# Kernel tuning notes

Measured on AMD Instinct MI355X. Metric: run time of the kernel, lower is better.

Reference implementation:

```python
import jax, jax.numpy as jnp
from jax import lax
import numpy as np

N_BLOCKS = 5; C = 256; K = 1024; NQ = 8; NRES = 4; B = 2; T = 65536


def conv1d(x, w, b, stride=1, padding=0, dilation=1):
    # x: [N,C,T], w: [O,I,k]
    y = lax.conv_general_dilated(x, w, (stride,), [(padding, padding)],
                                 rhs_dilation=(dilation,),
                                 dimension_numbers=('NCH', 'OIH', 'NCH'))
    return y + b[None, :, None]


def conv_transpose1d(x, w, b):
    # PyTorch ConvTranspose1d(k=4, s=2, p=1); w: [in, out, 4]
    wk = jnp.swapaxes(jnp.flip(w, -1), 0, 1)  # [out, in, 4]
    y = lax.conv_general_dilated(x, wk, (1,), [(2, 2)], lhs_dilation=(2,),
                                 dimension_numbers=('NCH', 'OIH', 'NCH'))
    return y + b[None, :, None]


def residual_model(x, w0, b0, w1, b1, dil):
    # ReLU -> dilated conv3 -> ReLU -> conv3
    h = conv1d(jax.nn.relu(x), w0, b0, padding=dil, dilation=dil)
    h = conv1d(jax.nn.relu(h), w1, b1, padding=1)
    return h


def encoder(x, d0w, d0b, dw, db, rw, rb):
    for i in range(N_BLOCKS):
        if i == 0:
            x = conv1d(x, d0w, d0b, stride=2, padding=1)
        else:
            x = conv1d(x, dw[i - 1], db[i - 1], stride=2, padding=1)
        for j in range(NRES):
            dil = 3 ** (j + 1)
            # ResidualBlock.forward: x + model(x)
            x = x + residual_model(x, rw[i, j, 0], rb[i, j, 0], rw[i, j, 1], rb[i, j, 1], dil)
    return x


def decoder(x, rw, rb, uw, ub, ulw, ulb):
    for i in range(N_BLOCKS):
        for j in range(NRES):
            dil = 3 ** (j + 1)
            # DecoderBlock: x = x + ResidualBlock(x) = x + (x + model(x))
            x = x + (x + residual_model(x, rw[i, j, 0], rb[i, j, 0], rw[i, j, 1], rb[i, j, 1], dil))
        if i == N_BLOCKS - 1:
            x = conv_transpose1d(x, ulw, ulb)
        else:
            x = conv_transpose1d(x, uw[i], ub[i])
    return x


def rvq(emb, rvq_sum, rvq_usage):
    # emb: [N, C]; eval-mode residual VQ (no EMA update)
    q = jnp.zeros_like(emb)
    commit = jnp.asarray(0.0, emb.dtype)
    codes = []
    for i in range(NQ):
        cb = rvq_sum[i] / jnp.clip(rvq_usage[i], 1e-5, None)[:, None]  # [K, C]
        res = emb - q
        # argmin of squared distance over codebook rows (||res||^2 constant per column)
        scores = jnp.sum(cb * cb, axis=1)[:, None] - 2.0 * (cb @ res.T)  # [K, N]
        c = jnp.argmin(scores, axis=0)
        eq = cb[c]  # [N, C]
        eq_st = res + lax.stop_gradient(eq - res)  # straight-through
        commit = commit + jnp.mean((lax.stop_gradient(eq_st) - res) ** 2)
        q = q + eq_st
        codes.append(c.astype(jnp.int32))
    return jnp.stack(codes, axis=1), q, commit


def setup_inputs() -> dict:
    key = jax.random.key(0)
    ks = iter(jax.random.split(key, 16))

    def W(shape, fan_in):
        return (jax.random.normal(next(ks), shape, jnp.float32) / np.float32(np.sqrt(fan_in)))

    return {
        'x': jax.random.normal(next(ks), (B, 1, T), jnp.float32),
        'enc_down0_w': W((C, 1, 4), 4),
        'enc_down0_b': jnp.zeros((C,), jnp.float32),
        'enc_down_w': W((N_BLOCKS - 1, C, C, 4), C * 4),
        'enc_down_b': jnp.zeros((N_BLOCKS - 1, C), jnp.float32),
        'enc_res_w': W((N_BLOCKS, NRES, 2, C, C, 3), C * 3),
        'enc_res_b': jnp.zeros((N_BLOCKS, NRES, 2, C), jnp.float32),
        'dec_res_w': W((N_BLOCKS, NRES, 2, C, C, 3), C * 3),
        'dec_res_b': jnp.zeros((N_BLOCKS, NRES, 2, C), jnp.float32),
        'dec_up_w': W((N_BLOCKS - 1, C, C, 4), C * 4),
        'dec_up_b': jnp.zeros((N_BLOCKS - 1, C), jnp.float32),
        'dec_up_last_w': W((C, 1, 4), C * 4),
        'dec_up_last_b': jnp.zeros((1,), jnp.float32),
        'rvq_sum': jax.random.normal(next(ks), (NQ, K, C), jnp.float32) * 0.1,
        'rvq_usage': jnp.ones((NQ, K), jnp.float32),
    }


def reference(x, enc_down0_w, enc_down0_b, enc_down_w, enc_down_b, enc_res_w, enc_res_b,
              dec_res_w, dec_res_b, dec_up_w, dec_up_b, dec_up_last_w, dec_up_last_b,
              rvq_sum, rvq_usage):
    z = encoder(x, enc_down0_w, enc_down0_b, enc_down_w, enc_down_b, enc_res_w, enc_res_b)
    Bz, Cz, Tz = z.shape
    emb = jnp.transpose(z, (0, 2, 1)).reshape(Bz * Tz, Cz)  # (b t) c
    codes, q, commit = rvq(emb, rvq_sum, rvq_usage)
    zq = jnp.transpose(q.reshape(Bz, Tz, Cz), (0, 2, 1))  # b c t
    recon = decoder(zq, dec_res_w, dec_res_b, dec_up_w, dec_up_b, dec_up_last_w, dec_up_last_b)
    return recon, codes, commit
```

## Files before the change

kernel.cpp:

```cpp
#include <hip/hip_runtime.h>
#include <cstdint>

#define DEVFN static __device__ __forceinline__
typedef unsigned short ushort_t;
typedef unsigned int uint_t;
typedef short short8 __attribute__((ext_vector_type(8)));
typedef float f32x4 __attribute__((ext_vector_type(4)));

DEVFN float bf2f(ushort_t h) { return __uint_as_float(((uint_t)h) << 16); }
DEVFN ushort_t bfhi(float f) {
    uint_t u = __float_as_uint(f);
    u += 0x7fffu + ((u >> 16) & 1u);
    return (ushort_t)(u >> 16);
}
DEVFN void fsplit(float f, ushort_t& h, ushort_t& l) {
    h = bfhi(f);
    l = bfhi(f - bf2f(h));
}
DEVFN void relu_pair(uint_t& h, uint_t& l) {
    float f0 = bf2f((ushort_t)(h & 0xffffu)) + bf2f((ushort_t)(l & 0xffffu));
    float f1 = bf2f((ushort_t)(h >> 16)) + bf2f((ushort_t)(l >> 16));
    if (f0 <= 0.f) { h &= 0xffff0000u; l &= 0xffff0000u; }
    if (f1 <= 0.f) { h &= 0x0000ffffu; l &= 0x0000ffffu; }
}
DEVFN int xcd_swz(int bx, int gx) {
    return ((gx & 7) == 0) ? ((bx & 7) * (gx >> 3) + (bx >> 3)) : bx;
}

__global__ __launch_bounds__(256)
void wprep3_k(const float* __restrict__ erw, const float* __restrict__ drw,
              ushort_t* __restrict__ wH, ushort_t* __restrict__ wL)
{
    const int gid = blockIdx.x * 256 + threadIdx.x;
    const int conv = gid >> 16;
    const int rem  = gid & 65535;
    const int co = rem >> 8, ci = rem & 255;
    const float* src = (conv < 40) ? (erw + (size_t)conv * 196608)
                                   : (drw + (size_t)(conv - 40) * 196608);
    const float* p = src + ((size_t)co * 256 + ci) * 3;
    ushort_t* oh = wH + (size_t)conv * 196608 + rem;
    ushort_t* ol = wL + (size_t)conv * 196608 + rem;
#pragma unroll
    for (int k = 0; k < 3; ++k) {
        ushort_t h, l; fsplit(p[k], h, l);
        oh[k * 65536] = h; ol[k * 65536] = l;
    }
}

__global__ __launch_bounds__(256)
void wprep4_k(const float* __restrict__ edw, const float* __restrict__ duw,
              ushort_t* __restrict__ wH, ushort_t* __restrict__ wL)
{
    const int gid = blockIdx.x * 256 + threadIdx.x;
    const int conv = gid >> 16;
    const int rem  = gid & 65535;
    const int co = rem >> 8, ci = rem & 255;
    ushort_t* oh = wH + (size_t)conv * 262144 + rem;
    ushort_t* ol = wL + (size_t)conv * 262144 + rem;
#pragma unroll
    for (int k = 0; k < 4; ++k) {
        float f;
        if (conv < 4)  f = edw[(size_t)conv * 262144 + ((size_t)co * 256 + ci) * 4 + k];
        else           f = duw[(size_t)(conv - 4) * 262144 + ((size_t)ci * 256 + co) * 4 + k];
        ushort_t h, l; fsplit(f, h, l);
        oh[k * 65536] = h; ol[k * 65536] = l;
    }
}

template<int TAPS, int STRIDE, bool RELU, int NT, int DMAX, bool DBUF>
__global__ __launch_bounds__(256, (NT >= 8) ? 2 : 3)
void convs_k(const ushort_t* __restrict__ inH, const ushort_t* __restrict__ inL,
             const ushort_t* __restrict__ wH, const ushort_t* __restrict__ wL,
             const float* __restrict__ bias,
             const ushort_t* __restrict__ srcH, const ushort_t* __restrict__ srcL,
             float alpha,
             ushort_t* __restrict__ outH, ushort_t* __restrict__ outL,
             int Lin, int Lout, int dil, int pad)
{
    constexpr int ROWS = NT * 16;
    constexpr int SMAX = STRIDE * (ROWS - 1) + (TAPS - 1) * DMAX + 1;
    constexpr int XSB  = SMAX * 80;
    constexpr int NEED = DBUF ? 4 * XSB : 2 * XSB;
    constexpr int EMIN = (NT >= 2) ? 33280 : 16640;
    constexpr int ARENA = (NEED > EMIN) ? NEED : EMIN;
    static_assert(!DBUF || (4 * SMAX <= TAPS * 256), "prefetch item budget");
    __shared__ __align__(16) char sarena[ARENA];

    const int tid = threadIdx.x;
    const int b = blockIdx.z;
    const int t0 = xcd_swz(blockIdx.x, gridDim.x) * ROWS;
    const int wave = tid >> 6, lane = tid & 63;
    const int quad = lane >> 4, lr = lane & 15;
    const int cow = wave * 64;
    const size_t inbase = (size_t)b * Lin * 256;
    const int S = STRIDE * (ROWS - 1) + (TAPS - 1) * dil + 1;
    const int g0 = STRIDE * t0 - pad;

    f32x4 acc[4][NT];
#pragma unroll
    for (int m = 0; m < 4; ++m)
#pragma unroll
        for (int n = 0; n < NT; ++n) acc[m][n] = (f32x4)0.f;

    if constexpr (DBUF) {
        ushort_t (*xsH0)[40] = (ushort_t(*)[40])(sarena);
        ushort_t (*xsL0)[40] = (ushort_t(*)[40])(sarena + XSB);
        ushort_t (*xsH1)[40] = (ushort_t(*)[40])(sarena + 2 * XSB);
        ushort_t (*xsL1)[40] = (ushort_t(*)[40])(sarena + 3 * XSB);
        for (int idx = tid; idx < S * 4; idx += 256) {
            const int s = idx >> 2, p = idx & 3;
            const int t = g0 + s;
            uint4 hv = make_uint4(0, 0, 0, 0), lv = hv;
            if (t >= 0 && t < Lin) {
                const size_t g = inbase + (size_t)t * 256 + p * 8;
                hv = *(const uint4*)(inH + g);
                lv = *(const uint4*)(inL + g);
                if (RELU) {
                    relu_pair(hv.x, lv.x); relu_pair(hv.y, lv.y);
                    relu_pair(hv.z, lv.z); relu_pair(hv.w, lv.w);
                }
            }
            *(uint4*)&xsH0[s][p * 8] = hv;
            *(uint4*)&xsL0[s][p * 8] = lv;
        }
        __syncthreads();
        for (int chunk = 0; chunk < 8; ++chunk) {
            const int ci0 = chunk * 32;
            ushort_t (*xsH)[40] = (chunk & 1) ? xsH1 : xsH0;
            ushort_t (*xsL)[40] = (chunk & 1) ? xsL1 : xsL0;
            ushort_t (*xnH)[40] = (chunk & 1) ? xsH0 : xsH1;
            ushort_t (*xnL)[40] = (chunk & 1) ? xsL0 : xsL1;
            const bool pf = (chunk < 7);
#pragma unroll
            for (int tap = 0; tap < TAPS; ++tap) {
                const ushort_t* wHt = wH + (size_t)tap * 65536 + ci0 + quad * 8;
                const ushort_t* wLt = wL + (size_t)tap * 65536 + ci0 + quad * 8;
                short8 aH[4], aL[4];
#pragma unroll
                for (int m = 0; m < 4; ++m) {
                    const int co = cow + m * 16 + lr;
                    aH[m] = *(const short8*)(wHt + co * 256);
                    aL[m] = *(const short8*)(wLt + co * 256);
                }
                const int idx = tap * 256 + tid;
                const int s = idx >> 2, p = idx & 3;
                const int tr = g0 + s;
                const bool inr = (idx < S * 4);
                uint4 hv = make_uint4(0, 0, 0, 0), lv = hv;
                if (pf && inr && tr >= 0 && tr < Lin) {
                    const size_t g = inbase + (size_t)tr * 256 + (ci0 + 32) + p * 8;
                    hv = *(const uint4*)(inH + g);
                    lv = *(const uint4*)(inL + g);
                }
                const int rb = tap * dil;
                __builtin_amdgcn_s_setprio(1);
#pragma unroll
                for (int n = 0; n < NT; ++n) {
                    const int srow = STRIDE * (n * 16 + lr) + rb;
                    const short8 bH = *(const short8*)&xsH[srow][quad * 8];
                    const short8 bL = *(const short8*)&xsL[srow][quad * 8];
#pragma unroll
                    for (int m = 0; m < 4; ++m)
                        acc[m][n] = __builtin_amdgcn_mfma_f32_16x16x32_bf16(aH[m], bH, acc[m][n], 0, 0, 0);
#pragma unroll
                    for (int m = 0; m < 4; ++m)
                        acc[m][n] = __builtin_amdgcn_mfma_f32_16x16x32_bf16(aH[m], bL, acc[m][n], 0, 0, 0);
#pragma unroll
                    for (int m = 0; m < 4; ++m)
                        acc[m][n] = __builtin_amdgcn_mfma_f32_16x16x32_bf16(aL[m], bH, acc[m][n], 0, 0, 0);
                }
                __builtin_amdgcn_s_setprio(0);
                if (pf && inr) {
                    if (RELU) {
                        relu_pair(hv.x, lv.x); relu_pair(hv.y, lv.y);
                        relu_pair(hv.z, lv.z); relu_pair(hv.w, lv.w);
                    }
                    *(uint4*)&xnH[s][p * 8] = hv;
                    *(uint4*)&xnL[s][p * 8] = lv;
                }
            }
            __syncthreads();
        }
    } else {
        ushort_t (*xsH)[40] = (ushort_t(*)[40])(sarena);
        ushort_t (*xsL)[40] = (ushort_t(*)[40])(sarena + XSB);
        for (int chunk = 0; chunk < 8; ++chunk) {
            const int ci0 = chunk * 32;
            __syncthreads();
            for (int idx = tid; idx < S * 4; idx += 256) {
                const int s = idx >> 2, p = idx & 3;
                const int t = g0 + s;
                uint4 hv = make_uint4(0, 0, 0, 0), lv = hv;
                if (t >= 0 && t < Lin) {
                    const size_t g = inbase + (size_t)t * 256 + ci0 + p * 8;
                    hv = *(const uint4*)(inH + g);
                    lv = *(const uint4*)(inL + g);
                    if (RELU) {
                        relu_pair(hv.x, lv.x); relu_pair(hv.y, lv.y);
                        relu_pair(hv.z, lv.z); relu_pair(hv.w, lv.w);
                    }
                }
                *(uint4*)&xsH[s][p * 8] = hv;
                *(uint4*)&xsL[s][p * 8] = lv;
            }
            __syncthreads();
#pragma unroll
            for (int tap = 0; tap < TAPS; ++tap) {
                const ushort_t* wHt = wH + (size_t)tap * 65536 + ci0 + quad * 8;
                const ushort_t* wLt = wL + (size_t)tap * 65536 + ci0 + quad * 8;
                short8 aH[4], aL[4];
#pragma unroll
                for (int m = 0; m < 4; ++m) {
                    const int co = cow + m * 16 + lr;
                    aH[m] = *(const short8*)(wHt + co * 256);
                    aL[m] = *(const short8*)(wLt + co * 256);
                }
                const int rb = tap * dil;
                __builtin_amdgcn_s_setprio(1);
#pragma unroll
                for (int n = 0; n < NT; ++n) {
                    const int srow = STRIDE * (n * 16 + lr) + rb;
                    const short8 bH = *(const short8*)&xsH[srow][quad * 8];
                    const short8 bL = *(const short8*)&xsL[srow][quad * 8];
#pragma unroll
                    for (int m = 0; m < 4; ++m)
                        acc[m][n] = __builtin_amdgcn_mfma_f32_16x16x32_bf16(aH[m], bH, acc[m][n], 0, 0, 0);
#pragma unroll
                    for (int m = 0; m < 4; ++m)
                        acc[m][n] = __builtin_amdgcn_mfma_f32_16x16x32_bf16(aH[m], bL, acc[m][n], 0, 0, 0);
#pragma unroll
                    for (int m = 0; m < 4; ++m)
                        acc[m][n] = __builtin_amdgcn_mfma_f32_16x16x32_bf16(aL[m], bH, acc[m][n], 0, 0, 0);
                }
                __builtin_amdgcn_s_setprio(0);
            }
        }
    }
    float4 bvv[4];
#pragma unroll
    for (int m = 0; m < 4; ++m)
        bvv[m] = *(const float4*)&bias[cow + m * 16 + quad * 4];
    __syncthreads();
    if constexpr (NT >= 2) {
        float (*ebuf)[260] = (float(*)[260])sarena;
#pragma unroll
        for (int n2 = 0; n2 < NT; n2 += 2) {
#pragma unroll
            for (int half = 0; half < 2; ++half) {
                const int n = n2 + half;
#pragma unroll
                for (int m = 0; m < 4; ++m) {
                    float4 v;
                    v.x = acc[m][n][0] + bvv[m].x;
                    v.y = acc[m][n][1] + bvv[m].y;
                    v.z = acc[m][n][2] + bvv[m].z;
                    v.w = acc[m][n][3] + bvv[m].w;
                    *(float4*)&ebuf[16 * half + lr][cow + m * 16 + quad * 4] = v;
                }
            }
            __syncthreads();
#pragma unroll
            for (int h = 0; h < 8; ++h) {
                const int row = (tid >> 4) + 16 * (h >> 2);
                const int col = (tid & 15) * 4 + (h & 3) * 64;
                const int t = t0 + n2 * 16 + row;
                const size_t gr = ((size_t)b * Lout + t) * 256;
                float4 v = *(const float4*)&ebuf[row][col];
                if (alpha != 0.f) {
                    const ushort4 sh = *(const ushort4*)(srcH + gr + col);
                    const ushort4 sl = *(const ushort4*)(srcL + gr + col);
                    v.x += alpha * (bf2f(sh.x) + bf2f(sl.x));
                    v.y += alpha * (bf2f(sh.y) + bf2f(sl.y));
                    v.z += alpha * (bf2f(sh.z) + bf2f(sl.z));
                    v.w += alpha * (bf2f(sh.w) + bf2f(sl.w));
                }
                ushort4 oh, ol;
                fsplit(v.x, oh.x, ol.x); fsplit(v.y, oh.y, ol.y);
                fsplit(v.z, oh.z, ol.z); fsplit(v.w, oh.w, ol.w);
                *(ushort4*)(outH + gr + col) = oh;
                *(ushort4*)(outL + gr + col) = ol;
            }
            __syncthreads();
        }
    } else {
        float (*ebuf)[260] = (float(*)[260])sarena;
#pragma unroll
        for (int n = 0; n < NT; ++n) {
#pragma unroll
            for (int m = 0; m < 4; ++m) {
                float4 v;
                v.x = acc[m][n][0] + bvv[m].x;
                v.y = acc[m][n][1] + bvv[m].y;
                v.z = acc[m][n][2] + bvv[m].z;
                v.w = acc[m][n][3] + bvv[m].w;
                *(float4*)&ebuf[lr][cow + m * 16 + quad * 4] = v;
            }
            __syncthreads();
            {
                const int row = tid >> 4;
                const int c00 = (tid & 15) * 4;
                const int t = t0 + n * 16 + row;
                const size_t gr = ((size_t)b * Lout + t) * 256;
#pragma unroll
                for (int rep = 0; rep < 4; ++rep) {
                    const int col = c00 + rep * 64;
                    float4 v = *(const float4*)&ebuf[row][col];
                    if (alpha != 0.f) {
                        const ushort4 sh = *(const ushort4*)(srcH + gr + col);
                        const ushort4 sl = *(const ushort4*)(srcL + gr + col);
                        v.x += alpha * (bf2f(sh.x) + bf2f(sl.x));
                        v.y += alpha * (bf2f(sh.y) + bf2f(sl.y));
                        v.z += alpha * (bf2f(sh.z) + bf2f(sl.z));
                        v.w += alpha * (bf2f(sh.w) + bf2f(sl.w));
                    }
                    ushort4 oh, ol;
                    fsplit(v.x, oh.x, ol.x); fsplit(v.y, oh.y, ol.y);
                    fsplit(v.z, oh.z, ol.z); fsplit(v.w, oh.w, ol.w);
                    *(ushort4*)(outH + gr + col) = oh;
                    *(ushort4*)(outL + gr + col) = ol;
                }
            }
            __syncthreads();
        }
    }
}

template<int NTc>
__global__ __launch_bounds__(256, 2)
void convt_k(const ushort_t* __restrict__ inH, const ushort_t* __restrict__ inL,
             const ushort_t* __restrict__ wH, const ushort_t* __restrict__ wL,
             const float* __restrict__ bias,
             ushort_t* __restrict__ outH, ushort_t* __restrict__ outL, int Lin)
{
    constexpr int ROWS = NTc * 16;
    constexpr int S = ROWS + 2;
    constexpr int XSB = S * 40 * 2;
    constexpr int ARENA = (2 * XSB > 33280) ? 2 * XSB : 33280;
    __shared__ __align__(16) char sarena[ARENA];
    ushort_t (*xsH)[40] = (ushort_t(*)[40])(sarena);
    ushort_t (*xsL)[40] = (ushort_t(*)[40])(sarena + XSB);

    const int tid = threadIdx.x;
    const int b = blockIdx.z;
    const int m0 = xcd_swz(blockIdx.x, gridDim.x) * ROWS;
    const int Lout = Lin * 2;
    const int wave = tid >> 6, lane = tid & 63;
    const int quad = lane >> 4, lr = lane & 15;
    const int cow = wave * 64;
    const size_t inbase = (size_t)b * Lin * 256;

    f32x4 acc[4][NTc][2];
#pragma unroll
    for (int m = 0; m < 4; ++m)
#pragma unroll
        for (int n = 0; n < NTc; ++n) { acc[m][n][0] = (f32x4)0.f; acc[m][n][1] = (f32x4)0.f; }

    for (int chunk = 0; chunk < 8; ++chunk) {
        const int ci0 = chunk * 32;
        __syncthreads();
        for (int idx = tid; idx < S * 4; idx += 256) {
            const int s = idx >> 2, p = idx & 3;
            const int t = m0 - 1 + s;
            uint4 hv = make_uint4(0, 0, 0, 0), lv = hv;
            if (t >= 0 && t < Lin) {
                const size_t g = inbase + (size_t)t * 256 + ci0 + p * 8;
                hv = *(const uint4*)(inH + g);
                lv = *(const uint4*)(inL + g);
            }
            *(uint4*)&xsH[s][p * 8] = hv;
            *(uint4*)&xsL[s][p * 8] = lv;
        }
        __syncthreads();
#pragma unroll
        for (int tap = 0; tap < 4; ++tap) {
            const int ph = (tap == 0 || tap == 2) ? 1 : 0;
            const int sh = (tap == 0) ? 1 : ((tap == 3) ? -1 : 0);
            const ushort_t* wHt = wH + (size_t)tap * 65536 + ci0 + quad * 8;
            const ushort_t* wLt = wL + (size_t)tap * 65536 + ci0 + quad * 8;
            short8 aH[4], aL[4];
#pragma unroll
            for (int m = 0; m < 4; ++m) {
                const int co = cow + m * 16 + lr;
                aH[m] = *(const short8*)(wHt + co * 256);
                aL[m] = *(const short8*)(wLt + co * 256);
            }
            __builtin_amdgcn_s_setprio(1);
#pragma unroll
            for (int n = 0; n < NTc; ++n) {
                const int srow = n * 16 + lr + sh + 1;
                const short8 bH = *(const short8*)&xsH[srow][quad * 8];
                const short8 bL = *(const short8*)&xsL[srow][quad * 8];
#pragma unroll
                for (int m = 0; m < 4; ++m)
                    acc[m][n][ph] = __builtin_amdgcn_mfma_f32_16x16x32_bf16(aH[m], bH, acc[m][n][ph], 0, 0, 0);
#pragma unroll
                for (int m = 0; m < 4; ++m)
                    acc[m][n][ph] = __builtin_amdgcn_mfma_f32_16x16x32_bf16(aH[m], bL, acc[m][n][ph], 0, 0, 0);
#pragma unroll
                for (int m = 0; m < 4; ++m)
                    acc[m][n][ph] = __builtin_amdgcn_mfma_f32_16x16x32_bf16(aL[m], bH, acc[m][n][ph], 0, 0, 0);
            }
            __builtin_amdgcn_s_setprio(0);
        }
    }
    float4 bvv[4];
#pragma unroll
    for (int m = 0; m < 4; ++m)
        bvv[m] = *(const float4*)&bias[cow + m * 16 + quad * 4];
    __syncthreads();
    float (*ebuf)[260] = (float(*)[260])sarena;
#pragma unroll
    for (int n = 0; n < NTc; ++n) {
#pragma unroll
        for (int m = 0; m < 4; ++m) {
#pragma unroll
            for (int ph = 0; ph < 2; ++ph) {
                float4 v;
                v.x = acc[m][n][ph][0] + bvv[m].x;
                v.y = acc[m][n][ph][1] + bvv[m].y;
                v.z = acc[m][n][ph][2] + bvv[m].z;
                v.w = acc[m][n][ph][3] + bvv[m].w;
                *(float4*)&ebuf[2 * lr + ph][cow + m * 16 + quad * 4] = v;
            }
        }
        __syncthreads();
        {
            const int baset = 2 * (m0 + n * 16);
#pragma unroll
            for (int h = 0; h < 8; ++h) {
                const int row = (tid >> 4) + 16 * (h >> 2);
                const int col = (tid & 15) * 4 + (h & 3) * 64;
                const int t = baset + row;
                const size_t gr = ((size_t)b * Lout + t) * 256 + col;
                float4 v = *(const float4*)&ebuf[row][col];
                ushort4 oh, ol;
                fsplit(v.x, oh.x, ol.x); fsplit(v.y, oh.y, ol.y);
                fsplit(v.z, oh.z, ol.z); fsplit(v.w, oh.w, ol.w);
                *(ushort4*)(outH + gr) = oh;
                *(ushort4*)(outL + gr) = ol;
            }
        }
        __syncthreads();
    }
}

__global__ __launch_bounds__(256)
void down0_k2(const float* __restrict__ x, const float* __restrict__ w,
              const float* __restrict__ bias,
              ushort_t* __restrict__ outH, ushort_t* __restrict__ outL)
{
    const int t = blockIdx.x;
    const int b = blockIdx.y;
    const int co = threadIdx.x;
    const float* xb = x + (size_t)b * 65536;
    const float4 wv = *(const float4*)(w + co * 4);
    float s = bias[co];
    const int ti0 = 2 * t - 1;
    if (ti0 >= 0)      s = fmaf(xb[ti0], wv.x, s);
    s = fmaf(xb[ti0 + 1], wv.y, s);
    s = fmaf(xb[ti0 + 2], wv.z, s);
    if (ti0 + 3 < 65536) s = fmaf(xb[ti0 + 3], wv.w, s);
    ushort_t h, l; fsplit(s, h, l);
    const size_t g = ((size_t)b * 32768 + t) * 256 + co;
    outH[g] = h; outL[g] = l;
}

__global__ __launch_bounds__(256)
void uplast_k2(const ushort_t* __restrict__ inH, const ushort_t* __restrict__ inL,
               const float* __restrict__ w, const float* __restrict__ bias,
               float* __restrict__ out, int Lin)
{
    const int m = blockIdx.x * 256 + threadIdx.x;
    const int b = blockIdx.y;
    const float bv = bias[0];
    float aE = bv, aO = bv;
    const size_t base = (size_t)b * Lin * 256;
    const ushort_t* r0H = inH + base + (size_t)m * 256;
    const ushort_t* r0L = inL + base + (size_t)m * 256;
    const bool hasM = (m > 0), hasP = (m + 1 < Lin);
    for (int c0 = 0; c0 < 256; c0 += 8) {
        uint4 h0 = *(const uint4*)(r0H + c0);
        uint4 l0 = *(const uint4*)(r0L + c0);
        uint4 hm = make_uint4(0,0,0,0), lm = hm, hp = hm, lp = hm;
        if (hasM) { hm = *(const uint4*)(r0H - 256 + c0); lm = *(const uint4*)(r0L - 256 + c0); }
        if (hasP) { hp = *(const uint4*)(r0H + 256 + c0); lp = *(const uint4*)(r0L + 256 + c0); }
        const uint_t* h0p = (const uint_t*)&h0; const uint_t* l0p = (const uint_t*)&l0;
        const uint_t* hmp = (const uint_t*)&hm; const uint_t* lmp = (const uint_t*)&lm;
        const uint_t* hpp = (const uint_t*)&hp; const uint_t* lpp = (const uint_t*)&lp;
#pragma unroll
        for (int e = 0; e < 4; ++e) {
#pragma unroll
            for (int half = 0; half < 2; ++half) {
                const int sh = half * 16;
                const int ci = c0 + e * 2 + half;
                const float x0  = bf2f((ushort_t)(h0p[e] >> sh)) + bf2f((ushort_t)(l0p[e] >> sh));
                const float xm1 = bf2f((ushort_t)(hmp[e] >> sh)) + bf2f((ushort_t)(lmp[e] >> sh));
                const float xp1 = bf2f((ushort_t)(hpp[e] >> sh)) + bf2f((ushort_t)(lpp[e] >> sh));
                const float4 wv = *(const float4*)(w + ci * 4);
                aE = fmaf(x0, wv.y, fmaf(xm1, wv.w, aE));
                aO = fmaf(xp1, wv.x, fmaf(x0, wv.z, aO));
            }
        }
    }
    *(float2*)(out + (size_t)b * 2 * Lin + 2 * m) = make_float2(aE, aO);
}

__global__ void emb_k(const ushort_t* __restrict__ H, const ushort_t* __restrict__ L,
                      float* __restrict__ emb)
{
    const size_t g = (size_t)blockIdx.x * 256 + threadIdx.x;
    emb[g] = bf2f(H[g]) + bf2f(L[g]);
}
__global__ void qsplit_k(const float* __restrict__ q,
                         ushort_t* __restrict__ H, ushort_t* __restrict__ L)
{
    const size_t g = (size_t)blockIdx.x * 256 + threadIdx.x;
    ushort_t h, l; fsplit(q[g], h, l);
    H[g] = h; L[g] = l;
}

__global__ __launch_bounds__(256)
void rvq_cb_all_k(const float* __restrict__ sum, const float* __restrict__ usage,
                  float* __restrict__ cb, float* __restrict__ cbT,
                  float* __restrict__ cbn)
{
    const int k = blockIdx.x, iq = blockIdx.y, c = threadIdx.x;
    const float den = fmaxf(usage[iq * 1024 + k], 1e-5f);
    const float v = sum[((size_t)iq * 1024 + k) * 256 + c] / den;
    cb[(size_t)iq * 262144 + (size_t)k * 256 + c] = v;
    cbT[(size_t)iq * 262144 + (size_t)c * 1024 + k] = v;
    float s = v * v;
    for (int off = 32; off; off >>= 1) s += __shfl_down(s, off, 64);
    __shared__ float ls[4];
    if ((c & 63) == 0) ls[c >> 6] = s;
    __syncthreads();
    if (c == 0) cbn[iq * 1024 + k] = ls[0] + ls[1] + ls[2] + ls[3];
}

DEVFN unsigned int ordbits(float f)
{
    unsigned u = __float_as_uint(f);
    return (u & 0x80000000u) ? ~u : (u | 0x80000000u);
}
DEVFN unsigned long long shfl_xor_u64(unsigned long long v, int mask)
{
    int lo = (int)(v & 0xffffffffull), hi = (int)(v >> 32);
    lo = __shfl_xor(lo, mask, 64);
    hi = __shfl_xor(hi, mask, 64);
    return ((unsigned long long)(unsigned)hi << 32) | (unsigned)lo;
}

__global__ __launch_bounds__(256)
void rvq_argmin_upd_k(const float* __restrict__ emb, float* __restrict__ q,
                      const float* __restrict__ cb, const float* __restrict__ cbT,
                      const float* __restrict__ cbn,
                      int* __restrict__ codes, float* __restrict__ codes_out,
                      float* __restrict__ commit, int iq)
{
    cb  += (size_t)iq * 262144;
    cbT += (size_t)iq * 262144;
    cbn += (size_t)iq * 1024;
    const int n0 = blockIdx.x * 16;
    const int tid = threadIdx.x;
    __shared__ float res[16][256];
    for (int idx = tid; idx < 16 * 256; idx += 256) {
        int nl = idx >> 8, c = idx & 255;
        size_t g = (size_t)(n0 + nl) * 256 + c;
        res[nl][c] = emb[g] - q[g];
    }
    __syncthreads();
    float dot[16][4];
#pragma unroll
    for (int nl = 0; nl < 16; ++nl)
#pragma unroll
        for (int j = 0; j < 4; ++j) dot[nl][j] = 0.f;

    const float* cbtp = cbT + tid * 4;
    for (int c = 0; c < 256; ++c) {
        const float4 cbv = *(const float4*)(cbtp + (size_t)c * 1024);
#pragma unroll
        for (int nl = 0; nl < 16; ++nl) {
            const float r = res[nl][c];
            dot[nl][0] = fmaf(cbv.x, r, dot[nl][0]);
            dot[nl][1] = fmaf(cbv.y, r, dot[nl][1]);
            dot[nl][2] = fmaf(cbv.z, r, dot[nl][2]);
            dot[nl][3] = fmaf(cbv.w, r, dot[nl][3]);
        }
    }
    const float4 nrm = *(const float4*)(cbn + tid * 4);
    __shared__ unsigned long long wred[4][16];
    __shared__ int scode[16];
    const int wave = tid >> 6, lane = tid & 63;
#pragma unroll
    for (int nl = 0; nl < 16; ++nl) {
        float s0 = nrm.x - 2.f * dot[nl][0];
        float s1 = nrm.y - 2.f * dot[nl][1];
        float s2 = nrm.z - 2.f * dot[nl][2];
        float s3 = nrm.w - 2.f * dot[nl][3];
        unsigned long long key =
            ((unsigned long long)ordbits(s0) << 32) | (unsigned)(tid * 4 + 0);
        unsigned long long k1 =
            ((unsigned long long)ordbits(s1) << 32) | (unsigned)(tid * 4 + 1);
        unsigned long long k2 =
            ((unsigned long long)ordbits(s2) << 32) | (unsigned)(tid * 4 + 2);
        unsigned long long k3 =
            ((unsigned long long)ordbits(s3) << 32) | (unsigned)(tid * 4 + 3);
        if (k1 < key) key = k1;
        if (k2 < key) key = k2;
        if (k3 < key) key = k3;
        for (int off = 32; off; off >>= 1) {
            unsigned long long o = shfl_xor_u64(key, off);
            if (o < key) key = o;
        }
        if (lane == 0) wred[wave][nl] = key;
    }
    __syncthreads();
    if (tid < 16) {
        unsigned long long bkey = wred[0][tid];
        if (wred[1][tid] < bkey) bkey = wred[1][tid];
        if (wred[2][tid] < bkey) bkey = wred[2][tid];
        if (wred[3][tid] < bkey) bkey = wred[3][tid];
        const int code = (int)(bkey & 0xffffffffull);
        scode[tid] = code;
        codes[(size_t)(n0 + tid) * 8 + iq] = code;
        codes_out[(size_t)(n0 + tid) * 8 + iq] = (float)code;
    }
    __syncthreads();
    float csum = 0.f;
#pragma unroll 4
    for (int nl = 0; nl < 16; ++nl) {
        const int code = scode[nl];
        const float cbv = cb[(size_t)code * 256 + tid];
        const float r = res[nl][tid];
        const size_t g = (size_t)(n0 + nl) * 256 + tid;
        q[g] = emb[g] - r + cbv;
        const float e = cbv - r;
        csum = fmaf(e, e, csum);
    }
    for (int off = 32; off; off >>= 1) csum += __shfl_down(csum, off, 64);
    __shared__ float ls2[4];
    if ((tid & 63) == 0) ls2[tid >> 6] = csum;
    __syncthreads();
    if (tid == 0) atomicAdd(commit, ls2[0] + ls2[1] + ls2[2] + ls2[3]);
}

__global__ void commit_write_k(const float* __restrict__ commit, float* __restrict__ out)
{
    out[0] = commit[0] * (1.f / (4096.f * 256.f));
}

extern "C" void kernel_launch(void* const* d_in, const int* in_sizes, int n_in,
                              void* d_out, int out_size, void* d_ws, size_t ws_size,
                              hipStream_t stream)
{
    const float* x    = (const float*)d_in[0];
    const float* ed0w = (const float*)d_in[1];
    const float* ed0b = (const float*)d_in[2];
    const float* edw  = (const float*)d_in[3];
    const float* edb  = (const float*)d_in[4];
    const float* erw  = (const float*)d_in[5];
    const float* erb  = (const float*)d_in[6];
    const float* drw  = (const float*)d_in[7];
    const float* drb  = (const float*)d_in[8];
    const float* duw  = (const float*)d_in[9];
    const float* dub  = (const float*)d_in[10];
    const float* dulw = (const float*)d_in[11];
    const float* dulb = (const float*)d_in[12];
    const float* rsum = (const float*)d_in[13];
    const float* rusg = (const float*)d_in[14];
    float* out = (float*)d_out;

    char* base = (char*)d_ws;
    size_t o = 0;
    ushort_t* wH3 = (ushort_t*)(base + o); o += 31457280;
    ushort_t* wL3 = (ushort_t*)(base + o); o += 31457280;
    ushort_t* w4H = (ushort_t*)(base + o); o += 4194304;
    ushort_t* w4L = (ushort_t*)(base + o); o += 4194304;
    ushort_t* AH  = (ushort_t*)(base + o); o += 33554432;
    ushort_t* AL  = (ushort_t*)(base + o); o += 33554432;
    ushort_t* BH  = (ushort_t*)(base + o); o += 33554432;
    ushort_t* BL  = (ushort_t*)(base + o); o += 33554432;
    float* emb    = (float*)(base + o);    o += 4194304;
    float* q      = (float*)(base + o);    o += 4194304;
    float* commit = (float*)(base + o);    o += 64;
    float* cb     = (float*)(base + o);    o += 8388608;
    float* cbT    = (float*)(base + o);    o += 8388608;
    float* cbn    = (float*)(base + o);    o += 32768;
    int*   codes  = (int*)(base + o);      o += 131072;

    static const int DIL[4] = {3, 9, 27, 81};

    hipMemsetAsync(q, 0, 4194304 + 64, stream);

    wprep3_k<<<20480, 256, 0, stream>>>(erw, drw, wH3, wL3);
    wprep4_k<<<2048, 256, 0, stream>>>(edw, duw, w4H, w4L);

    auto conv3 = [&](const ushort_t* iH, const ushort_t* iL,
                     const ushort_t* wh, const ushort_t* wl, const float* bb,
                     const ushort_t* sH, const ushort_t* sL, float alpha,
                     ushort_t* oH, ushort_t* oL, int L, int d) {
        const bool db = (d <= 27);
        if (L >= 16384) {
            if (db) convs_k<3, 1, true, 8, 27, true><<<dim3(L / 128, 1, 2), 256, 0, stream>>>(
                        iH, iL, wh, wl, bb, sH, sL, alpha, oH, oL, L, L, d, d);
            else    convs_k<3, 1, true, 8, 81, false><<<dim3(L / 128, 1, 2), 256, 0, stream>>>(
                        iH, iL, wh, wl, bb, sH, sL, alpha, oH, oL, L, L, d, d);
        } else if (L >= 8192) {
            if (db) convs_k<3, 1, true, 4, 27, true><<<dim3(L / 64, 1, 2), 256, 0, stream>>>(
                        iH, iL, wh, wl, bb, sH, sL, alpha, oH, oL, L, L, d, d);
            else    convs_k<3, 1, true, 4, 81, false><<<dim3(L / 64, 1, 2), 256, 0, stream>>>(
                        iH, iL, wh, wl, bb, sH, sL, alpha, oH, oL, L, L, d, d);
        } else if (L >= 4096) {
            if (db) convs_k<3, 1, true, 2, 27, true><<<dim3(L / 32, 1, 2), 256, 0, stream>>>(
                        iH, iL, wh, wl, bb, sH, sL, alpha, oH, oL, L, L, d, d);
            else    convs_k<3, 1, true, 2, 81, false><<<dim3(L / 32, 1, 2), 256, 0, stream>>>(
                        iH, iL, wh, wl, bb, sH, sL, alpha, oH, oL, L, L, d, d);
        } else {
            if (db) convs_k<3, 1, true, 1, 27, true><<<dim3(L / 16, 1, 2), 256, 0, stream>>>(
                        iH, iL, wh, wl, bb, sH, sL, alpha, oH, oL, L, L, d, d);
            else    convs_k<3, 1, true, 1, 81, false><<<dim3(L / 16, 1, 2), 256, 0, stream>>>(
                        iH, iL, wh, wl, bb, sH, sL, alpha, oH, oL, L, L, d, d);
        }
    };

    down0_k2<<<dim3(32768, 2), 256, 0, stream>>>(x, ed0w, ed0b, AH, AL);
    int L = 32768;
    for (int i = 0; i < 5; ++i) {
        if (i > 0) {
            const ushort_t* wh = w4H + (size_t)(i - 1) * 262144;
            const ushort_t* wl = w4L + (size_t)(i - 1) * 262144;
            const int Lout = L / 2;
            if (Lout >= 16384)
                convs_k<4, 2, false, 8, 1, false><<<dim3(Lout / 128, 1, 2), 256, 0, stream>>>(
                    AH, AL, wh, wl, edb + (i - 1) * 256, AH, AL, 0.f, BH, BL, L, Lout, 1, 1);
            else if (Lout >= 8192)
                convs_k<4, 2, false, 4, 1, false><<<dim3(Lout / 64, 1, 2), 256, 0, stream>>>(
                    AH, AL, wh, wl, edb + (i - 1) * 256, AH, AL, 0.f, BH, BL, L, Lout, 1, 1);
            else if (Lout >= 4096)
                convs_k<4, 2, false, 2, 1, false><<<dim3(Lout / 32, 1, 2), 256, 0, stream>>>(
                    AH, AL, wh, wl, edb + (i - 1) * 256, AH, AL, 0.f, BH, BL, L, Lout, 1, 1);
            else
                convs_k<4, 2, false, 1, 1, false><<<dim3(Lout / 16, 1, 2), 256, 0, stream>>>(
                    AH, AL, wh, wl, edb + (i - 1) * 256, AH, AL, 0.f, BH, BL, L, Lout, 1, 1);
            ushort_t* t;
            t = AH; AH = BH; BH = t;
            t = AL; AL = BL; BL = t;
            L = Lout;
        }
        for (int j = 0; j < 4; ++j) {
            const int d = DIL[j];
            const size_t u = (size_t)(i * 4 + j) * 2;
            conv3(AH, AL, wH3 + (u + 0) * 196608, wL3 + (u + 0) * 196608,
                  erb + (u + 0) * 256, AH, AL, 0.f, BH, BL, L, d);
            conv3(BH, BL, wH3 + (u + 1) * 196608, wL3 + (u + 1) * 196608,
                  erb + (u + 1) * 256, AH, AL, 1.f, AH, AL, L, 1);
        }
    }

    emb_k<<<4096, 256, 0, stream>>>(AH, AL, emb);
    rvq_cb_all_k<<<dim3(1024, 8), 256, 0, stream>>>(rsum, rusg, cb, cbT, cbn);
    for (int iq = 0; iq < 8; ++iq) {
        rvq_argmin_upd_k<<<256, 256, 0, stream>>>(emb, q, cb, cbT, cbn,
                                                  codes, out + 131072, commit, iq);
    }
    qsplit_k<<<4096, 256, 0, stream>>>(q, AH, AL);

    L = 2048;
    for (int i = 0; i < 5; ++i) {
        for (int j = 0; j < 4; ++j) {
            const int d = DIL[j];
            const size_t u = 40 + (size_t)(i * 4 + j) * 2;
            conv3(AH, AL, wH3 + (u + 0) * 196608, wL3 + (u + 0) * 196608,
                  drb + ((size_t)(i * 4 + j) * 2 + 0) * 256, AH, AL, 0.f, BH, BL, L, d);
            conv3(BH, BL, wH3 + (u + 1) * 196608, wL3 + (u + 1) * 196608,
                  drb + ((size_t)(i * 4 + j) * 2 + 1) * 256, AH, AL, 2.f, AH, AL, L, 1);
        }
        if (i < 4) {
            const ushort_t* wh = w4H + (size_t)(4 + i) * 262144;
            const ushort_t* wl = w4L + (size_t)(4 + i) * 262144;
            if (L >= 8192)
                convt_k<4><<<dim3(L / 64, 1, 2), 256, 0, stream>>>(
                    AH, AL, wh, wl, dub + i * 256, BH, BL, L);
            else if (L >= 4096)
                convt_k<2><<<dim3(L / 32, 1, 2), 256, 0, stream>>>(
                    AH, AL, wh, wl, dub + i * 256, BH, BL, L);
            else
                convt_k<1><<<dim3(L / 16, 1, 2), 256, 0, stream>>>(
                    AH, AL, wh, wl, dub + i * 256, BH, BL, L);
            ushort_t* t;
            t = AH; AH = BH; BH = t;
            t = AL; AL = BL; BL = t;
            L *= 2;
        } else {
            uplast_k2<<<dim3(L / 256, 2), 256, 0, stream>>>(AH, AL, dulw, dulb, out, L);
        }
    }

    commit_write_k<<<1, 1, 0, stream>>>(commit, out + 163840);
}
```

Measured before the change: 5.277 ms.

## Fuse all RVQ stages into one kernel keeping residual in shared memory

Replaces the emb conversion kernel, the eight per-stage argmin/update launches and the q split kernel with a single kernel that loads the encoder output once, keeps the residual and quantized accumulator in shared memory across all eight codebook stages, and writes the split bf16 pair back at the end. This removes the repeated global reads and writes of emb and q and nine kernel launches. It also changes the dilated conv3 dispatch so the small-dilation variant uses the 8-wide tile only at L>=32768 and the 4-wide tile at 16384. Shared memory per block doubles, and the 32-bit codes buffer is no longer written.

```diff
diff --git a/kernel.cpp b/kernel.cpp
--- a/kernel.cpp
+++ b/kernel.cpp
@@ -505,20 +505,6 @@
     *(float2*)(out + (size_t)b * 2 * Lin + 2 * m) = make_float2(aE, aO);
 }
 
-__global__ void emb_k(const ushort_t* __restrict__ H, const ushort_t* __restrict__ L,
-                      float* __restrict__ emb)
-{
-    const size_t g = (size_t)blockIdx.x * 256 + threadIdx.x;
-    emb[g] = bf2f(H[g]) + bf2f(L[g]);
-}
-__global__ void qsplit_k(const float* __restrict__ q,
-                         ushort_t* __restrict__ H, ushort_t* __restrict__ L)
-{
-    const size_t g = (size_t)blockIdx.x * 256 + threadIdx.x;
-    ushort_t h, l; fsplit(q[g], h, l);
-    H[g] = h; L[g] = l;
-}
-
 __global__ __launch_bounds__(256)
 void rvq_cb_all_k(const float* __restrict__ sum, const float* __restrict__ usage,
                   float* __restrict__ cb, float* __restrict__ cbT,
@@ -551,97 +537,114 @@
 }
 
 __global__ __launch_bounds__(256)
-void rvq_argmin_upd_k(const float* __restrict__ emb, float* __restrict__ q,
-                      const float* __restrict__ cb, const float* __restrict__ cbT,
-                      const float* __restrict__ cbn,
-                      int* __restrict__ codes, float* __restrict__ codes_out,
-                      float* __restrict__ commit, int iq)
-{
-    cb  += (size_t)iq * 262144;
-    cbT += (size_t)iq * 262144;
-    cbn += (size_t)iq * 1024;
+void rvq_all_k(ushort_t* __restrict__ AH, ushort_t* __restrict__ AL,
+               const float* __restrict__ cb, const float* __restrict__ cbT,
+               const float* __restrict__ cbn,
+               float* __restrict__ codes_out, float* __restrict__ commit)
+{
     const int n0 = blockIdx.x * 16;
     const int tid = threadIdx.x;
     __shared__ float res[16][256];
-    for (int idx = tid; idx < 16 * 256; idx += 256) {
-        int nl = idx >> 8, c = idx & 255;
-        size_t g = (size_t)(n0 + nl) * 256 + c;
-        res[nl][c] = emb[g] - q[g];
-    }
-    __syncthreads();
-    float dot[16][4];
-#pragma unroll
-    for (int nl = 0; nl < 16; ++nl)
-#pragma unroll
-        for (int j = 0; j < 4; ++j) dot[nl][j] = 0.f;
-
-    const float* cbtp = cbT + tid * 4;
-    for (int c = 0; c < 256; ++c) {
-        const float4 cbv = *(const float4*)(cbtp + (size_t)c * 1024);
-#pragma unroll
-        for (int nl = 0; nl < 16; ++nl) {
-            const float r = res[nl][c];
-            dot[nl][0] = fmaf(cbv.x, r, dot[nl][0]);
-            dot[nl][1] = fmaf(cbv.y, r, dot[nl][1]);
-            dot[nl][2] = fmaf(cbv.z, r, dot[nl][2]);
-            dot[nl][3] = fmaf(cbv.w, r, dot[nl][3]);
-        }
-    }
-    const float4 nrm = *(const float4*)(cbn + tid * 4);
+    __shared__ float qacc[16][256];
     __shared__ unsigned long long wred[4][16];
     __shared__ int scode[16];
+    for (int idx = tid; idx < 1024; idx += 256) {
+        const int nl = idx >> 6, c4 = (idx & 63) * 4;
+        const size_t g = (size_t)(n0 + nl) * 256 + c4;
+        const ushort4 h = *(const ushort4*)(AH + g);
+        const ushort4 l = *(const ushort4*)(AL + g);
+        res[nl][c4 + 0] = bf2f(h.x) + bf2f(l.x);
+        res[nl][c4 + 1] = bf2f(h.y) + bf2f(l.y);
+        res[nl][c4 + 2] = bf2f(h.z) + bf2f(l.z);
+        res[nl][c4 + 3] = bf2f(h.w) + bf2f(l.w);
+        qacc[nl][c4 + 0] = 0.f; qacc[nl][c4 + 1] = 0.f;
+        qacc[nl][c4 + 2] = 0.f; qacc[nl][c4 + 3] = 0.f;
+    }
+    __syncthreads();
     const int wave = tid >> 6, lane = tid & 63;
-#pragma unroll
-    for (int nl = 0; nl < 16; ++nl) {
-        float s0 = nrm.x - 2.f * dot[nl][0];
-        float s1 = nrm.y - 2.f * dot[nl][1];
-        float s2 = nrm.z - 2.f * dot[nl][2];
-        float s3 = nrm.w - 2.f * dot[nl][3];
-        unsigned long long key =
-            ((unsigned long long)ordbits(s0) << 32) | (unsigned)(tid * 4 + 0);
-        unsigned long long k1 =
-            ((unsigned long long)ordbits(s1) << 32) | (unsigned)(tid * 4 + 1);
-        unsigned long long k2 =
-            ((unsigned long long)ordbits(s2) << 32) | (unsigned)(tid * 4 + 2);
-        unsigned long long k3 =
-            ((unsigned long long)ordbits(s3) << 32) | (unsigned)(tid * 4 + 3);
-        if (k1 < key) key = k1;
-        if (k2 < key) key = k2;
-        if (k3 < key) key = k3;
-        for (int off = 32; off; off >>= 1) {
-            unsigned long long o = shfl_xor_u64(key, off);
-            if (o < key) key = o;
-        }
-        if (lane == 0) wred[wave][nl] = key;
-    }
-    __syncthreads();
-    if (tid < 16) {
-        unsigned long long bkey = wred[0][tid];
-        if (wred[1][tid] < bkey) bkey = wred[1][tid];
-        if (wred[2][tid] < bkey) bkey = wred[2][tid];
-        if (wred[3][tid] < bkey) bkey = wred[3][tid];
-        const int code = (int)(bkey & 0xffffffffull);
-        scode[tid] = code;
-        codes[(size_t)(n0 + tid) * 8 + iq] = code;
-        codes_out[(size_t)(n0 + tid) * 8 + iq] = (float)code;
-    }
-    __syncthreads();
     float csum = 0.f;
+    for (int iq = 0; iq < 8; ++iq) {
+        const float* cbq  = cb  + (size_t)iq * 262144;
+        const float* cbtp = cbT + (size_t)iq * 262144 + tid * 4;
+        float dot[16][4];
+#pragma unroll
+        for (int nl = 0; nl < 16; ++nl)
+#pragma unroll
+            for (int j = 0; j < 4; ++j) dot[nl][j] = 0.f;
+        for (int c = 0; c < 256; ++c) {
+            const float4 cbv = *(const float4*)(cbtp + (size_t)c * 1024);
+#pragma unroll
+            for (int nl = 0; nl < 16; ++nl) {
+                const float r = res[nl][c];
+                dot[nl][0] = fmaf(cbv.x, r, dot[nl][0]);
+                dot[nl][1] = fmaf(cbv.y, r, dot[nl][1]);
+                dot[nl][2] = fmaf(cbv.z, r, dot[nl][2]);
+                dot[nl][3] = fmaf(cbv.w, r, dot[nl][3]);
+            }
+        }
+        const float4 nrm = *(const float4*)(cbn + iq * 1024 + tid * 4);
+#pragma unroll
+        for (int nl = 0; nl < 16; ++nl) {
+            float s0 = nrm.x - 2.f * dot[nl][0];
+            float s1 = nrm.y - 2.f * dot[nl][1];
+            float s2 = nrm.z - 2.f * dot[nl][2];
+            float s3 = nrm.w - 2.f * dot[nl][3];
+            unsigned long long key =
+                ((unsigned long long)ordbits(s0) << 32) | (unsigned)(tid * 4 + 0);
+            unsigned long long k1 =
+                ((unsigned long long)ordbits(s1) << 32) | (unsigned)(tid * 4 + 1);
+            unsigned long long k2 =
+                ((unsigned long long)ordbits(s2) << 32) | (unsigned)(tid * 4 + 2);
+            unsigned long long k3 =
+                ((unsigned long long)ordbits(s3) << 32) | (unsigned)(tid * 4 + 3);
+            if (k1 < key) key = k1;
+            if (k2 < key) key = k2;
+            if (k3 < key) key = k3;
+            for (int off = 32; off; off >>= 1) {
+                unsigned long long o = shfl_xor_u64(key, off);
+                if (o < key) key = o;
+            }
+            if (lane == 0) wred[wave][nl] = key;
+        }
+        __syncthreads();
+        if (tid < 16) {
+            unsigned long long bkey = wred[0][tid];
+            if (wred[1][tid] < bkey) bkey = wred[1][tid];
+            if (wred[2][tid] < bkey) bkey = wred[2][tid];
+            if (wred[3][tid] < bkey) bkey = wred[3][tid];
+            const int code = (int)(bkey & 0xffffffffull);
+            scode[tid] = code;
+            codes_out[(size_t)(n0 + tid) * 8 + iq] = (float)code;
+        }
+        __syncthreads();
 #pragma unroll 4
-    for (int nl = 0; nl < 16; ++nl) {
-        const int code = scode[nl];
-        const float cbv = cb[(size_t)code * 256 + tid];
-        const float r = res[nl][tid];
-        const size_t g = (size_t)(n0 + nl) * 256 + tid;
-        q[g] = emb[g] - r + cbv;
-        const float e = cbv - r;
-        csum = fmaf(e, e, csum);
+        for (int nl = 0; nl < 16; ++nl) {
+            const int code = scode[nl];
+            const float cbv = cbq[(size_t)code * 256 + tid];
+            const float r = res[nl][tid];
+            const float e = cbv - r;
+            csum = fmaf(e, e, csum);
+            res[nl][tid] = -e;
+            qacc[nl][tid] += cbv;
+        }
+        __syncthreads();
     }
     for (int off = 32; off; off >>= 1) csum += __shfl_down(csum, off, 64);
     __shared__ float ls2[4];
     if ((tid & 63) == 0) ls2[tid >> 6] = csum;
     __syncthreads();
     if (tid == 0) atomicAdd(commit, ls2[0] + ls2[1] + ls2[2] + ls2[3]);
+    for (int idx = tid; idx < 1024; idx += 256) {
+        const int nl = idx >> 6, c4 = (idx & 63) * 4;
+        const size_t g = (size_t)(n0 + nl) * 256 + c4;
+        ushort4 oh, ol;
+        fsplit(qacc[nl][c4 + 0], oh.x, ol.x);
+        fsplit(qacc[nl][c4 + 1], oh.y, ol.y);
+        fsplit(qacc[nl][c4 + 2], oh.z, ol.z);
+        fsplit(qacc[nl][c4 + 3], oh.w, ol.w);
+        *(ushort4*)(AH + g) = oh;
+        *(ushort4*)(AL + g) = ol;
+    }
 }
 
 __global__ void commit_write_k(const float* __restrict__ commit, float* __restrict__ out)
@@ -680,17 +683,14 @@
     ushort_t* AL  = (ushort_t*)(base + o); o += 33554432;
     ushort_t* BH  = (ushort_t*)(base + o); o += 33554432;
     ushort_t* BL  = (ushort_t*)(base + o); o += 33554432;
-    float* emb    = (float*)(base + o);    o += 4194304;
-    float* q      = (float*)(base + o);    o += 4194304;
     float* commit = (float*)(base + o);    o += 64;
     float* cb     = (float*)(base + o);    o += 8388608;
     float* cbT    = (float*)(base + o);    o += 8388608;
     float* cbn    = (float*)(base + o);    o += 32768;
-    int*   codes  = (int*)(base + o);      o += 131072;
 
     static const int DIL[4] = {3, 9, 27, 81};
 
-    hipMemsetAsync(q, 0, 4194304 + 64, stream);
+    hipMemsetAsync(commit, 0, 64, stream);
 
     wprep3_k<<<20480, 256, 0, stream>>>(erw, drw, wH3, wL3);
     wprep4_k<<<2048, 256, 0, stream>>>(edw, duw, w4H, w4L);
@@ -700,26 +700,32 @@
                      const ushort_t* sH, const ushort_t* sL, float alpha,
                      ushort_t* oH, ushort_t* oL, int L, int d) {
         const bool db = (d <= 27);
-        if (L >= 16384) {
-            if (db) convs_k<3, 1, true, 8, 27, true><<<dim3(L / 128, 1, 2), 256, 0, stream>>>(
-                        iH, iL, wh, wl, bb, sH, sL, alpha, oH, oL, L, L, d, d);
-            else    convs_k<3, 1, true, 8, 81, false><<<dim3(L / 128, 1, 2), 256, 0, stream>>>(
-                        iH, iL, wh, wl, bb, sH, sL, alpha, oH, oL, L, L, d, d);
-        } else if (L >= 8192) {
-            if (db) convs_k<3, 1, true, 4, 27, true><<<dim3(L / 64, 1, 2), 256, 0, stream>>>(
-                        iH, iL, wh, wl, bb, sH, sL, alpha, oH, oL, L, L, d, d);
-            else    convs_k<3, 1, true, 4, 81, false><<<dim3(L / 64, 1, 2), 256, 0, stream>>>(
-                        iH, iL, wh, wl, bb, sH, sL, alpha, oH, oL, L, L, d, d);
-        } else if (L >= 4096) {
-            if (db) convs_k<3, 1, true, 2, 27, true><<<dim3(L / 32, 1, 2), 256, 0, stream>>>(
-                        iH, iL, wh, wl, bb, sH, sL, alpha, oH, oL, L, L, d, d);
-            else    convs_k<3, 1, true, 2, 81, false><<<dim3(L / 32, 1, 2), 256, 0, stream>>>(
-                        iH, iL, wh, wl, bb, sH, sL, alpha, oH, oL, L, L, d, d);
+        if (db) {
+            if (L >= 32768)
+                convs_k<3, 1, true, 8, 27, true><<<dim3(L / 128, 1, 2), 256, 0, stream>>>(
+                    iH, iL, wh, wl, bb, sH, sL, alpha, oH, oL, L, L, d, d);
+            else if (L >= 8192)
+                convs_k<3, 1, true, 4, 27, true><<<dim3(L / 64, 1, 2), 256, 0, stream>>>(
+                    iH, iL, wh, wl, bb, sH, sL, alpha, oH, oL, L, L, d, d);
+            else if (L >= 4096)
+                convs_k<3, 1, true, 2, 27, true><<<dim3(L / 32, 1, 2), 256, 0, stream>>>(
+                    iH, iL, wh, wl, bb, sH, sL, alpha, oH, oL, L, L, d, d);
+            else
+                convs_k<3, 1, true, 1, 27, true><<<dim3(L / 16, 1, 2), 256, 0, stream>>>(
+                    iH, iL, wh, wl, bb, sH, sL, alpha, oH, oL, L, L, d, d);
         } else {
-            if (db) convs_k<3, 1, true, 1, 27, true><<<dim3(L / 16, 1, 2), 256, 0, stream>>>(
-                        iH, iL, wh, wl, bb, sH, sL, alpha, oH, oL, L, L, d, d);
-            else    convs_k<3, 1, true, 1, 81, false><<<dim3(L / 16, 1, 2), 256, 0, stream>>>(
-                        iH, iL, wh, wl, bb, sH, sL, alpha, oH, oL, L, L, d, d);
+            if (L >= 16384)
+                convs_k<3, 1, true, 8, 81, false><<<dim3(L / 128, 1, 2), 256, 0, stream>>>(
+                    iH, iL, wh, wl, bb, sH, sL, alpha, oH, oL, L, L, d, d);
+            else if (L >= 8192)
+                convs_k<3, 1, true, 4, 81, false><<<dim3(L / 64, 1, 2), 256, 0, stream>>>(
+                    iH, iL, wh, wl, bb, sH, sL, alpha, oH, oL, L, L, d, d);
+            else if (L >= 4096)
+                convs_k<3, 1, true, 2, 81, false><<<dim3(L / 32, 1, 2), 256, 0, stream>>>(
+                    iH, iL, wh, wl, bb, sH, sL, alpha, oH, oL, L, L, d, d);
+            else
+                convs_k<3, 1, true, 1, 81, false><<<dim3(L / 16, 1, 2), 256, 0, stream>>>(
+                    iH, iL, wh, wl, bb, sH, sL, alpha, oH, oL, L, L, d, d);
         }
     };
 
@@ -757,13 +763,8 @@
         }
     }
 
-    emb_k<<<4096, 256, 0, stream>>>(AH, AL, emb);
     rvq_cb_all_k<<<dim3(1024, 8), 256, 0, stream>>>(rsum, rusg, cb, cbT, cbn);
-    for (int iq = 0; iq < 8; ++iq) {
-        rvq_argmin_upd_k<<<256, 256, 0, stream>>>(emb, q, cb, cbT, cbn,
-                                                  codes, out + 131072, commit, iq);
-    }
-    qsplit_k<<<4096, 256, 0, stream>>>(q, AH, AL);
+    rvq_all_k<<<256, 256, 0, stream>>>(AH, AL, cb, cbT, cbn, out + 131072, commit);
 
     L = 2048;
     for (int i = 0; i < 5; ++i) {
```

Result: no change. 5.201 ms (-1.4%).
